# Kernel optimization log

Hardware: AMD Instinct MI355X
Metric: run time of the kernel (lower is better)

Reference implementation:

```python
import jax, jax.numpy as jnp
import numpy as np

N, D, H = 8192, 256, 128
KEEP_RATIO = 0.5
TEMP = 1.0
COS_EPS = 1e-4  # torch CosineSimilarity eps
NEG = -9e15


def setup_inputs() -> dict:
    key = jax.random.key(0)
    k1, k2, k3, k4 = jax.random.split(key, 4)
    features = jax.random.normal(k1, (N, D), dtype=jnp.float32)
    adj = jax.random.randint(k2, (N, N), 0, 2, dtype=jnp.int32)
    # module init: Linear weights ~ N(0, 0.001)
    Wq = jax.random.normal(k3, (H, D), dtype=jnp.float32) * 0.001
    Wk = jax.random.normal(k4, (H, D), dtype=jnp.float32) * 0.001
    return {"features": features, "adj": adj, "Wq": Wq, "Wk": Wk}


def _cos_normalize(x):
    # torch cosine: x / max(||x||, eps)
    n = jnp.linalg.norm(x, axis=-1, keepdims=True)
    return x / jnp.maximum(n, COS_EPS)


def reference(features, adj, Wq, Wk):
    # projections [N, H]
    Qn = _cos_normalize(features @ Wq.T)
    Kn = _cos_normalize(features @ Wk.T)
    # raw_att[i, j] = cos(Wq f_j, Wk f_i)  -> [N, N]
    raw_att = Kn @ Qn.T
    att = jnp.where(adj > 0, raw_att, NEG) * TEMP
    att = jax.nn.softmax(att, axis=1)
    prop_fea = att @ features  # [N, D]
    # nodes with no neighbors keep their own features
    adj_mask = (jnp.sum(adj, axis=1) > 0).astype(features.dtype)[:, None]
    prop_fea = adj_mask * prop_fea + (1.0 - adj_mask) * features
    # gate=None branch: fixed keep_ratio mixing
    return (1.0 - KEEP_RATIO) * prop_fea + KEEP_RATIO * features
```

## Files before the change

kernel.cpp:

```cpp
#include <hip/hip_runtime.h>
#include <stdint.h>
#include <stddef.h>

#define NN 8192
#define DD 256
#define HH 128

typedef short bf16x8  __attribute__((ext_vector_type(8)));
typedef float f32x4   __attribute__((ext_vector_type(4)));
typedef float f32x16  __attribute__((ext_vector_type(16)));
typedef int   i32x4   __attribute__((ext_vector_type(4)));

static __device__ __forceinline__ short f2bf(float x){
  unsigned u = __float_as_uint(x);
  u = (u + 0x7FFFu + ((u >> 16) & 1u)) >> 16;
  return (short)(unsigned short)u;
}
static __device__ __forceinline__ bf16x8 cvt8(const float* p){
  f32x4 a = *(const f32x4*)p;
  f32x4 b = *(const f32x4*)(p + 4);
  bf16x8 o;
  o[0]=f2bf(a[0]); o[1]=f2bf(a[1]); o[2]=f2bf(a[2]); o[3]=f2bf(a[3]);
  o[4]=f2bf(b[0]); o[5]=f2bf(b[1]); o[6]=f2bf(b[2]); o[7]=f2bf(b[3]);
  return o;
}
static __device__ __forceinline__ bf16x8 ld16(const void* p){
  i32x4 v = *(const i32x4*)p;
  return __builtin_bit_cast(bf16x8, v);
}

__global__ __launch_bounds__(256) void k_ftfrag(const float* __restrict__ f,
                                                unsigned short* __restrict__ ftf){
  int t = threadIdx.x;
  int fr = blockIdx.x * 4 + (t >> 6);
  int l  = t & 63;
  int jt = fr >> 3, dt = fr & 7;
  int j = jt * 16 + (l >> 5) * 8, d = dt * 32 + (l & 31);
  bf16x8 o;
  #pragma unroll
  for (int e = 0; e < 8; ++e) o[e] = f2bf(f[(size_t)(j + e) * DD + d]);
  *(bf16x8*)(ftf + (size_t)fr * 512 + l * 8) = o;
}

__global__ __launch_bounds__(256) void k_proj(const float* __restrict__ f,
                                              const float* __restrict__ Wq,
                                              const float* __restrict__ Wk,
                                              unsigned short* __restrict__ Qnf,
                                              unsigned short* __restrict__ Kn){
  int t = threadIdx.x, wave = t >> 6, l = t & 63;
  int i0 = blockIdx.x * 64 + wave * 16;
  int lr = l & 15, lk = l >> 4;
  bf16x8 ka[8];
  #pragma unroll
  for (int ks = 0; ks < 8; ++ks)
    ka[ks] = cvt8(f + (size_t)(i0 + lr) * DD + ks * 32 + lk * 8);
  for (int pj = 0; pj < 2; ++pj){
    const float* W = pj ? Wk : Wq;
    f32x4 acc[8];
    #pragma unroll
    for (int n = 0; n < 8; ++n) acc[n] = (f32x4){0.f,0.f,0.f,0.f};
    for (int ks = 0; ks < 8; ++ks)
      #pragma unroll
      for (int n = 0; n < 8; ++n){
        bf16x8 bb = cvt8(W + (size_t)(n * 16 + lr) * DD + ks * 32 + lk * 8);
        acc[n] = __builtin_amdgcn_mfma_f32_16x16x32_bf16(ka[ks], bb, acc[n], 0, 0, 0);
      }
    #pragma unroll
    for (int r = 0; r < 4; ++r){
      float n2 = 0.f;
      #pragma unroll
      for (int n = 0; n < 8; ++n){ float v = acc[n][r]; n2 += v * v; }
      n2 += __shfl_xor(n2, 1); n2 += __shfl_xor(n2, 2);
      n2 += __shfl_xor(n2, 4); n2 += __shfl_xor(n2, 8);
      float s = 1.f / fmaxf(sqrtf(n2), 1e-4f);
      int row = i0 + lk * 4 + r;
      #pragma unroll
      for (int n = 0; n < 8; ++n){
        short v = f2bf(acc[n][r] * s);
        if (pj){
          Kn[(size_t)row * HH + n * 16 + lr] = (unsigned short)v;
        } else {
          size_t off = ((size_t)(row >> 5) * 8 + n) * 512
                     + ((row & 31) + 32 * (lr >> 3)) * 8 + (lr & 7);
          Qnf[off] = (unsigned short)v;
        }
      }
    }
  }
}

#define STEP(CUR, NXT, SS) {                                                      \
  const int j0 = jbase + (SS) * 64;                                               \
  const int jn = ((SS) < 31) ? j0 + 64 : j0;                                      \
  _Pragma("unroll")                                                               \
  for (int r = 0; r < 16; ++r)                                                    \
    NXT[r] = __builtin_nontemporal_load(                                          \
        adj + (size_t)(iA + (r & 3) + 8 * (r >> 2)) * NN + jn + jg * 32 + lc);    \
  f32x16 st;                                                                      \
  _Pragma("unroll") for (int e = 0; e < 16; ++e) st[e] = 0.f;                     \
  { const unsigned short* qb = Qnf + ((size_t)((j0 + jg * 32) >> 5) * 8) * 512 + (size_t)l * 8; \
    _Pragma("unroll")                                                             \
    for (int hs = 0; hs < 8; ++hs)                                                \
      st = __builtin_amdgcn_mfma_f32_32x32x16_bf16(kb[hs], ld16(qb + hs * 512), st, 0, 0, 0); } \
  bf16x8 bv[8];                                                                   \
  { const unsigned short* fb = ftf + ((size_t)(j0 >> 4) * 8 + wq * 2) * 512 + (size_t)l * 8; \
    _Pragma("unroll")                                                             \
    for (int ks = 0; ks < 4; ++ks){                                               \
      bv[ks * 2]     = ld16(fb + ks * 4096);                                      \
      bv[ks * 2 + 1] = ld16(fb + ks * 4096 + 512); } }                            \
  _Pragma("unroll")                                                               \
  for (int r = 0; r < 16; ++r){                                                   \
    float wv = (CUR[r] > 0) ? __expf(st[r]) : 0.f;          \
    dacc[r] += wv;                                                                \
    int row = ig * 32 + (r & 3) + 8 * (r >> 2) + 4 * h;                           \
    int byo = row * 128 + (((jg * 32 + lc) * 2) ^ ((row & 7) << 4));              \
    *(unsigned short*)(p_lds + byo) = (unsigned short)f2bf(wv);                   \
  }                                                                               \
  __syncthreads();                                                                \
  _Pragma("unroll")                                                               \
  for (int ks = 0; ks < 4; ++ks){                                                 \
    int ko = (ks * 32 + h * 16) ^ ((lc & 7) << 4);                                \
    bf16x8 pa0 = ld16(p_lds + lc * 128 + ko);                                     \
    bf16x8 pa1 = ld16(p_lds + (32 + lc) * 128 + ko);                              \
    pv00 = __builtin_amdgcn_mfma_f32_32x32x16_bf16(pa0, bv[ks*2],   pv00, 0,0,0); \
    pv01 = __builtin_amdgcn_mfma_f32_32x32x16_bf16(pa0, bv[ks*2+1], pv01, 0,0,0); \
    pv10 = __builtin_amdgcn_mfma_f32_32x32x16_bf16(pa1, bv[ks*2],   pv10, 0,0,0); \
    pv11 = __builtin_amdgcn_mfma_f32_32x32x16_bf16(pa1, bv[ks*2+1], pv11, 0,0,0); \
  }                                                                               \
  __syncthreads();                                                                \
}

__global__ __launch_bounds__(256, 2) void k_attn(
      const int* __restrict__ adj,
      const unsigned short* __restrict__ Qnf, const unsigned short* __restrict__ Kn,
      const unsigned short* __restrict__ ftf,
      float* __restrict__ num_p, float* __restrict__ den_p){
  __shared__ __attribute__((aligned(16))) char p_lds[8192];
  int t = threadIdx.x, wave = t >> 6, l = t & 63;
  int lc = l & 31, h = l >> 5;
  int ig = wave >> 1, jg = wave & 1, wq = wave;
  int ib = blockIdx.x >> 2, js = blockIdx.x & 3;
  int i0 = ib * 64;
  int jbase = js * 2048;
  int iA = i0 + ig * 32 + 4 * h;

  bf16x8 kb[8];
  { const unsigned short* kp = Kn + (size_t)(i0 + ig * 32 + lc) * HH + h * 8;
    #pragma unroll
    for (int hs = 0; hs < 8; ++hs) kb[hs] = ld16(kp + hs * 16); }

  f32x16 pv00, pv01, pv10, pv11;
  #pragma unroll
  for (int e = 0; e < 16; ++e){ pv00[e]=0.f; pv01[e]=0.f; pv10[e]=0.f; pv11[e]=0.f; }
  float dacc[16];
  #pragma unroll
  for (int r = 0; r < 16; ++r) dacc[r] = 0.f;

  int adjA[16], adjB[16];
  #pragma unroll
  for (int r = 0; r < 16; ++r)
    adjA[r] = __builtin_nontemporal_load(
        adj + (size_t)(iA + (r & 3) + 8 * (r >> 2)) * NN + jbase + jg * 32 + lc);

  for (int sp = 0; sp < 16; ++sp){
    STEP(adjA, adjB, 2 * sp)
    STEP(adjB, adjA, 2 * sp + 1)
  }

  #pragma unroll
  for (int r = 0; r < 16; ++r){
    float v = dacc[r];
    v += __shfl_xor(v, 1); v += __shfl_xor(v, 2); v += __shfl_xor(v, 4);
    v += __shfl_xor(v, 8); v += __shfl_xor(v, 16);
    if (lc == 0){
      int i = i0 + ig * 32 + (r & 3) + 8 * (r >> 2) + 4 * h;
      den_p[(size_t)(js * 2 + jg) * NN + i] = v;
    }
  }
  float* np = num_p + (size_t)js * NN * DD;
  #pragma unroll
  for (int r = 0; r < 16; ++r){
    int i = i0 + (r & 3) + 8 * (r >> 2) + 4 * h;
    int d = wq * 64 + lc;
    np[(size_t)i * DD + d]             = pv00[r];
    np[(size_t)i * DD + d + 32]        = pv01[r];
    np[(size_t)(i + 32) * DD + d]      = pv10[r];
    np[(size_t)(i + 32) * DD + d + 32] = pv11[r];
  }
}

__global__ __launch_bounds__(256) void k_final(const float* __restrict__ num_p,
                                               const float* __restrict__ den_p,
                                               const float* __restrict__ f,
                                               float* __restrict__ out){
  int gid = blockIdx.x * 256 + threadIdx.x;
  int i = gid >> 6;
  f32x4 nv = (f32x4){0.f,0.f,0.f,0.f};
  float dv = 0.f;
  #pragma unroll
  for (int s = 0; s < 4; ++s)
    nv += *(const f32x4*)(num_p + (size_t)s * NN * DD + (size_t)gid * 4);
  #pragma unroll
  for (int s = 0; s < 8; ++s)
    dv += den_p[(size_t)s * NN + i];
  f32x4 fv = *(const f32x4*)(f + (size_t)gid * 4);
  f32x4 o;
  if (dv > 0.f){
    float inv = 0.5f / dv;
    o = nv * inv + fv * 0.5f;
  } else {
    o = fv;
  }
  *(f32x4*)(out + (size_t)gid * 4) = o;
}

extern "C" void kernel_launch(void* const* d_in, const int* in_sizes, int n_in,
                              void* d_out, int out_size, void* d_ws, size_t ws_size,
                              hipStream_t stream){
  (void)in_sizes; (void)n_in; (void)out_size;
  const float* feat = (const float*)d_in[0];
  const int*   adj  = (const int*)d_in[1];
  const float* Wq   = (const float*)d_in[2];
  const float* Wk   = (const float*)d_in[3];
  float* out = (float*)d_out;
  char* ws = (char*)d_ws;
  unsigned short* Qnf  = (unsigned short*)(ws);
  unsigned short* Kn   = (unsigned short*)(ws + (2u << 20));
  unsigned short* ftf  = (unsigned short*)(ws + (4u << 20));
  float*          num_p = (float*)(ws + (8u << 20));
  float*          den_p = (float*)(ws + (40u << 20));
  if (ws_size < (40u << 20) + 262144u) return;

  k_ftfrag<<<1024, 256, 0, stream>>>(feat, ftf);
  k_proj<<<128, 256, 0, stream>>>(feat, Wq, Wk, Qnf, Kn);
  k_attn<<<512, 256, 0, stream>>>(adj, Qnf, Kn, ftf, num_p, den_p);
  k_final<<<2048, 256, 0, stream>>>(num_p, den_p, feat, out);
}
```

Before: 235.6 us.

## Stage adjacency tiles through double-buffered LDS with 16-byte vector loads

Adjacency tiles are now loaded with 128-bit nontemporal vector loads by all threads in a coalesced pattern and staged through a double-buffered LDS tile. Previously each thread issued sixteen scalar 4-byte loads per step in the MFMA output layout. The Q operand is now loaded before the score MFMAs rather than inline, and the step macro becomes a plain loop. This is meant to cut load-instruction count and improve coalescing on the dominant adjacency stream (256 MB of int32). In exchange it adds 32 KB of LDS per block, which may reduce occupancy, and adds LDS read/write traffic.

Result: faster. 219.9 us (-6.7%).

```diff
diff --git a/kernel.cpp b/kernel.cpp
--- a/kernel.cpp
+++ b/kernel.cpp
@@ -89,60 +89,19 @@
   }
 }
 
-#define STEP(CUR, NXT, SS) {                                                      \
-  const int j0 = jbase + (SS) * 64;                                               \
-  const int jn = ((SS) < 31) ? j0 + 64 : j0;                                      \
-  _Pragma("unroll")                                                               \
-  for (int r = 0; r < 16; ++r)                                                    \
-    NXT[r] = __builtin_nontemporal_load(                                          \
-        adj + (size_t)(iA + (r & 3) + 8 * (r >> 2)) * NN + jn + jg * 32 + lc);    \
-  f32x16 st;                                                                      \
-  _Pragma("unroll") for (int e = 0; e < 16; ++e) st[e] = 0.f;                     \
-  { const unsigned short* qb = Qnf + ((size_t)((j0 + jg * 32) >> 5) * 8) * 512 + (size_t)l * 8; \
-    _Pragma("unroll")                                                             \
-    for (int hs = 0; hs < 8; ++hs)                                                \
-      st = __builtin_amdgcn_mfma_f32_32x32x16_bf16(kb[hs], ld16(qb + hs * 512), st, 0, 0, 0); } \
-  bf16x8 bv[8];                                                                   \
-  { const unsigned short* fb = ftf + ((size_t)(j0 >> 4) * 8 + wq * 2) * 512 + (size_t)l * 8; \
-    _Pragma("unroll")                                                             \
-    for (int ks = 0; ks < 4; ++ks){                                               \
-      bv[ks * 2]     = ld16(fb + ks * 4096);                                      \
-      bv[ks * 2 + 1] = ld16(fb + ks * 4096 + 512); } }                            \
-  _Pragma("unroll")                                                               \
-  for (int r = 0; r < 16; ++r){                                                   \
-    float wv = (CUR[r] > 0) ? __expf(st[r]) : 0.f;          \
-    dacc[r] += wv;                                                                \
-    int row = ig * 32 + (r & 3) + 8 * (r >> 2) + 4 * h;                           \
-    int byo = row * 128 + (((jg * 32 + lc) * 2) ^ ((row & 7) << 4));              \
-    *(unsigned short*)(p_lds + byo) = (unsigned short)f2bf(wv);                   \
-  }                                                                               \
-  __syncthreads();                                                                \
-  _Pragma("unroll")                                                               \
-  for (int ks = 0; ks < 4; ++ks){                                                 \
-    int ko = (ks * 32 + h * 16) ^ ((lc & 7) << 4);                                \
-    bf16x8 pa0 = ld16(p_lds + lc * 128 + ko);                                     \
-    bf16x8 pa1 = ld16(p_lds + (32 + lc) * 128 + ko);                              \
-    pv00 = __builtin_amdgcn_mfma_f32_32x32x16_bf16(pa0, bv[ks*2],   pv00, 0,0,0); \
-    pv01 = __builtin_amdgcn_mfma_f32_32x32x16_bf16(pa0, bv[ks*2+1], pv01, 0,0,0); \
-    pv10 = __builtin_amdgcn_mfma_f32_32x32x16_bf16(pa1, bv[ks*2],   pv10, 0,0,0); \
-    pv11 = __builtin_amdgcn_mfma_f32_32x32x16_bf16(pa1, bv[ks*2+1], pv11, 0,0,0); \
-  }                                                                               \
-  __syncthreads();                                                                \
-}
-
 __global__ __launch_bounds__(256, 2) void k_attn(
       const int* __restrict__ adj,
       const unsigned short* __restrict__ Qnf, const unsigned short* __restrict__ Kn,
       const unsigned short* __restrict__ ftf,
       float* __restrict__ num_p, float* __restrict__ den_p){
   __shared__ __attribute__((aligned(16))) char p_lds[8192];
+  __shared__ __attribute__((aligned(16))) int adj_lds[2][64][64];
   int t = threadIdx.x, wave = t >> 6, l = t & 63;
   int lc = l & 31, h = l >> 5;
   int ig = wave >> 1, jg = wave & 1, wq = wave;
   int ib = blockIdx.x >> 2, js = blockIdx.x & 3;
   int i0 = ib * 64;
   int jbase = js * 2048;
-  int iA = i0 + ig * 32 + 4 * h;
 
   bf16x8 kb[8];
   { const unsigned short* kp = Kn + (size_t)(i0 + ig * 32 + lc) * HH + h * 8;
@@ -156,15 +115,76 @@
   #pragma unroll
   for (int r = 0; r < 16; ++r) dacc[r] = 0.f;
 
-  int adjA[16], adjB[16];
-  #pragma unroll
-  for (int r = 0; r < 16; ++r)
-    adjA[r] = __builtin_nontemporal_load(
-        adj + (size_t)(iA + (r & 3) + 8 * (r >> 2)) * NN + jbase + jg * 32 + lc);
-
-  for (int sp = 0; sp < 16; ++sp){
-    STEP(adjA, adjB, 2 * sp)
-    STEP(adjB, adjA, 2 * sp + 1)
+  int arow = wave * 16 + (l >> 4);
+  int acol = (l & 15) * 4;
+
+  #pragma unroll
+  for (int k4 = 0; k4 < 4; ++k4){
+    i32x4 v = __builtin_nontemporal_load(
+        (const i32x4*)(adj + (size_t)(i0 + arow + k4 * 4) * NN + jbase + acol));
+    *(i32x4*)&adj_lds[0][arow + k4 * 4][acol] = v;
+  }
+  __syncthreads();
+
+  for (int s = 0; s < 32; ++s){
+    int j0 = jbase + s * 64;
+    int cur = s & 1, nxt = cur ^ 1;
+
+    bf16x8 qv[8];
+    { const unsigned short* qb = Qnf + ((size_t)((j0 + jg * 32) >> 5) * 8) * 512 + (size_t)l * 8;
+      #pragma unroll
+      for (int hs = 0; hs < 8; ++hs) qv[hs] = ld16(qb + hs * 512); }
+
+    i32x4 av[4];
+    if (s < 31){
+      #pragma unroll
+      for (int k4 = 0; k4 < 4; ++k4)
+        av[k4] = __builtin_nontemporal_load(
+            (const i32x4*)(adj + (size_t)(i0 + arow + k4 * 4) * NN + j0 + 64 + acol));
+    }
+
+    bf16x8 bv[8];
+    { const unsigned short* fb = ftf + ((size_t)(j0 >> 4) * 8 + wq * 2) * 512 + (size_t)l * 8;
+      #pragma unroll
+      for (int ks = 0; ks < 4; ++ks){
+        bv[ks * 2]     = ld16(fb + ks * 4096);
+        bv[ks * 2 + 1] = ld16(fb + ks * 4096 + 512); } }
+
+    f32x16 st;
+    #pragma unroll
+    for (int e = 0; e < 16; ++e) st[e] = 0.f;
+    #pragma unroll
+    for (int hs = 0; hs < 8; ++hs)
+      st = __builtin_amdgcn_mfma_f32_32x32x16_bf16(kb[hs], qv[hs], st, 0, 0, 0);
+
+    #pragma unroll
+    for (int r = 0; r < 16; ++r){
+      int row = ig * 32 + (r & 3) + 8 * (r >> 2) + 4 * h;
+      int a = adj_lds[cur][row][jg * 32 + lc];
+      float wv = (a > 0) ? __expf(st[r]) : 0.f;
+      dacc[r] += wv;
+      int byo = row * 128 + (((jg * 32 + lc) * 2) ^ ((row & 7) << 4));
+      *(unsigned short*)(p_lds + byo) = (unsigned short)f2bf(wv);
+    }
+    __syncthreads();
+
+    if (s < 31){
+      #pragma unroll
+      for (int k4 = 0; k4 < 4; ++k4)
+        *(i32x4*)&adj_lds[nxt][arow + k4 * 4][acol] = av[k4];
+    }
+
+    #pragma unroll
+    for (int ks = 0; ks < 4; ++ks){
+      int ko = (ks * 32 + h * 16) ^ ((lc & 7) << 4);
+      bf16x8 pa0 = ld16(p_lds + lc * 128 + ko);
+      bf16x8 pa1 = ld16(p_lds + (32 + lc) * 128 + ko);
+      pv00 = __builtin_amdgcn_mfma_f32_32x32x16_bf16(pa0, bv[ks*2],   pv00, 0,0,0);
+      pv01 = __builtin_amdgcn_mfma_f32_32x32x16_bf16(pa0, bv[ks*2+1], pv01, 0,0,0);
+      pv10 = __builtin_amdgcn_mfma_f32_32x32x16_bf16(pa1, bv[ks*2],   pv10, 0,0,0);
+      pv11 = __builtin_amdgcn_mfma_f32_32x32x16_bf16(pa1, bv[ks*2+1], pv11, 0,0,0);
+    }
+    __syncthreads();
   }
 
   #pragma unroll
```

## Stage adjacency and Kn through LDS, prefetch Q fragments, fuse prep kernels

Applied to the files above, without the earlier changes.

The attention kernel now loads adjacency tiles with 16-byte vector loads into a double-buffered LDS tile instead of scalar per-lane loads, and moves Kn into swizzled LDS rather than holding it in registers. Q fragments for the next step are prefetched into registers. The ftf conversion and projection kernels are merged into one launch, with the W tiles staged through LDS. Together these cut global load instruction count and one launch, at the cost of more LDS use (about 56KB per block), which may hurt the two-blocks-per-CU occupancy.

Measured after the change: 203.8 us. 13.5% less time.

```diff
diff --git a/kernel.cpp b/kernel.cpp
--- a/kernel.cpp
+++ b/kernel.cpp
@@ -29,25 +29,25 @@
   return __builtin_bit_cast(bf16x8, v);
 }
 
-__global__ __launch_bounds__(256) void k_ftfrag(const float* __restrict__ f,
-                                                unsigned short* __restrict__ ftf){
-  int t = threadIdx.x;
-  int fr = blockIdx.x * 4 + (t >> 6);
-  int l  = t & 63;
-  int jt = fr >> 3, dt = fr & 7;
-  int j = jt * 16 + (l >> 5) * 8, d = dt * 32 + (l & 31);
-  bf16x8 o;
-  #pragma unroll
-  for (int e = 0; e < 8; ++e) o[e] = f2bf(f[(size_t)(j + e) * DD + d]);
-  *(bf16x8*)(ftf + (size_t)fr * 512 + l * 8) = o;
-}
-
-__global__ __launch_bounds__(256) void k_proj(const float* __restrict__ f,
+__global__ __launch_bounds__(256) void k_prep(const float* __restrict__ f,
                                               const float* __restrict__ Wq,
                                               const float* __restrict__ Wk,
+                                              unsigned short* __restrict__ ftf,
                                               unsigned short* __restrict__ Qnf,
                                               unsigned short* __restrict__ Kn){
-  int t = threadIdx.x, wave = t >> 6, l = t & 63;
+  __shared__ unsigned short wb[128][40];
+  int t = threadIdx.x, l = t & 63;
+  {
+    int fr = blockIdx.x * 4 + (t >> 6);
+    int jt = fr >> 3, dt = fr & 7;
+    int j = jt * 16 + (l >> 5) * 8, d = dt * 32 + (l & 31);
+    bf16x8 o;
+    #pragma unroll
+    for (int e = 0; e < 8; ++e) o[e] = f2bf(f[(size_t)(j + e) * DD + d]);
+    *(bf16x8*)(ftf + (size_t)fr * 512 + l * 8) = o;
+  }
+  if (blockIdx.x >= 128) return;
+  int wave = t >> 6;
   int i0 = blockIdx.x * 64 + wave * 16;
   int lr = l & 15, lk = l >> 4;
   bf16x8 ka[8];
@@ -59,12 +59,20 @@
     f32x4 acc[8];
     #pragma unroll
     for (int n = 0; n < 8; ++n) acc[n] = (f32x4){0.f,0.f,0.f,0.f};
-    for (int ks = 0; ks < 8; ++ks)
+    for (int ks = 0; ks < 8; ++ks){
+      __syncthreads();
+      { int row = t >> 1, c0 = (t & 1) * 16;
+        const float* wp = W + (size_t)row * DD + ks * 32 + c0;
+        bf16x8 w0 = cvt8(wp), w1 = cvt8(wp + 8);
+        *(bf16x8*)&wb[row][c0]     = w0;
+        *(bf16x8*)&wb[row][c0 + 8] = w1; }
+      __syncthreads();
       #pragma unroll
       for (int n = 0; n < 8; ++n){
-        bf16x8 bb = cvt8(W + (size_t)(n * 16 + lr) * DD + ks * 32 + lk * 8);
+        bf16x8 bb = ld16(&wb[n * 16 + lr][lk * 8]);
         acc[n] = __builtin_amdgcn_mfma_f32_16x16x32_bf16(ka[ks], bb, acc[n], 0, 0, 0);
       }
+    }
     #pragma unroll
     for (int r = 0; r < 4; ++r){
       float n2 = 0.f;
@@ -89,34 +97,51 @@
   }
 }
 
-#define STEP(CUR, NXT, SS) {                                                      \
-  const int j0 = jbase + (SS) * 64;                                               \
-  const int jn = ((SS) < 31) ? j0 + 64 : j0;                                      \
-  _Pragma("unroll")                                                               \
-  for (int r = 0; r < 16; ++r)                                                    \
-    NXT[r] = __builtin_nontemporal_load(                                          \
-        adj + (size_t)(iA + (r & 3) + 8 * (r >> 2)) * NN + jn + jg * 32 + lc);    \
-  f32x16 st;                                                                      \
-  _Pragma("unroll") for (int e = 0; e < 16; ++e) st[e] = 0.f;                     \
-  { const unsigned short* qb = Qnf + ((size_t)((j0 + jg * 32) >> 5) * 8) * 512 + (size_t)l * 8; \
-    _Pragma("unroll")                                                             \
-    for (int hs = 0; hs < 8; ++hs)                                                \
-      st = __builtin_amdgcn_mfma_f32_32x32x16_bf16(kb[hs], ld16(qb + hs * 512), st, 0, 0, 0); } \
+#define STEPX(CUR, NXT, QA, QB, S) {                                              \
+  const int j0 = jbase + (S) * 64;                                                \
+  const int jn = ((S) < 31) ? j0 + 64 : jbase;                                    \
+                       \
+  i32x4 av0 = __builtin_nontemporal_load((const i32x4*)(adj + (size_t)(i0 + arow) * NN + jn + acol));      \
+  i32x4 av1 = __builtin_nontemporal_load((const i32x4*)(adj + (size_t)(i0 + arow + 4) * NN + jn + acol));  \
+  i32x4 av2 = __builtin_nontemporal_load((const i32x4*)(adj + (size_t)(i0 + arow + 8) * NN + jn + acol));  \
+  i32x4 av3 = __builtin_nontemporal_load((const i32x4*)(adj + (size_t)(i0 + arow + 12) * NN + jn + acol)); \
+                                         \
   bf16x8 bv[8];                                                                   \
   { const unsigned short* fb = ftf + ((size_t)(j0 >> 4) * 8 + wq * 2) * 512 + (size_t)l * 8; \
     _Pragma("unroll")                                                             \
     for (int ks = 0; ks < 4; ++ks){                                               \
       bv[ks * 2]     = ld16(fb + ks * 4096);                                      \
       bv[ks * 2 + 1] = ld16(fb + ks * 4096 + 512); } }                            \
+                      \
+  f32x16 st;                                                                      \
+  _Pragma("unroll") for (int e = 0; e < 16; ++e) st[e] = 0.f;                     \
+  _Pragma("unroll")                                                               \
+  for (int hs = 0; hs < 8; ++hs){                                                 \
+    bf16x8 kv = ld16(kn_lds + klrow * 256 + ((hs * 32 + h * 16) ^ kswz));         \
+    st = __builtin_amdgcn_mfma_f32_32x32x16_bf16(kv, QA[hs], st, 0, 0, 0);        \
+  }                                                                               \
+        \
+  { const unsigned short* qp = Qnf + ((size_t)((jn + jg * 32) >> 5) * 8) * 512 + (size_t)l * 8; \
+    _Pragma("unroll")                                                             \
+    for (int hs = 0; hs < 8; ++hs) QB[hs] = ld16(qp + hs * 512); }                \
+                                            \
   _Pragma("unroll")                                                               \
   for (int r = 0; r < 16; ++r){                                                   \
-    float wv = (CUR[r] > 0) ? __expf(st[r]) : 0.f;          \
+    int row = ig * 32 + (r & 3) + 8 * (r >> 2) + 4 * h;                           \
+    int a = *(const int*)(adj_lds + (CUR) * 16384 + row * 256 + (jg * 32 + lc) * 4); \
+    float wv = (a > 0) ? __expf(st[r]) : 0.f;               \
     dacc[r] += wv;                                                                \
-    int row = ig * 32 + (r & 3) + 8 * (r >> 2) + 4 * h;                           \
     int byo = row * 128 + (((jg * 32 + lc) * 2) ^ ((row & 7) << 4));              \
     *(unsigned short*)(p_lds + byo) = (unsigned short)f2bf(wv);                   \
   }                                                                               \
-  __syncthreads();                                                                \
+  asm volatile("s_waitcnt lgkmcnt(0)" ::: "memory");   \
+  __builtin_amdgcn_s_barrier();                                                   \
+        \
+  *(i32x4*)(adj_lds + (NXT) * 16384 + arow * 256 + acol * 4)        = av0;        \
+  *(i32x4*)(adj_lds + (NXT) * 16384 + (arow + 4) * 256 + acol * 4)  = av1;        \
+  *(i32x4*)(adj_lds + (NXT) * 16384 + (arow + 8) * 256 + acol * 4)  = av2;        \
+  *(i32x4*)(adj_lds + (NXT) * 16384 + (arow + 12) * 256 + acol * 4) = av3;        \
+                                                    \
   _Pragma("unroll")                                                               \
   for (int ks = 0; ks < 4; ++ks){                                                 \
     int ko = (ks * 32 + h * 16) ^ ((lc & 7) << 4);                                \
@@ -127,7 +152,8 @@
     pv10 = __builtin_amdgcn_mfma_f32_32x32x16_bf16(pa1, bv[ks*2],   pv10, 0,0,0); \
     pv11 = __builtin_amdgcn_mfma_f32_32x32x16_bf16(pa1, bv[ks*2+1], pv11, 0,0,0); \
   }                                                                               \
-  __syncthreads();                                                                \
+  asm volatile("s_waitcnt lgkmcnt(0)" ::: "memory");   \
+  __builtin_amdgcn_s_barrier();                                                   \
 }
 
 __global__ __launch_bounds__(256, 2) void k_attn(
@@ -136,18 +162,25 @@
       const unsigned short* __restrict__ ftf,
       float* __restrict__ num_p, float* __restrict__ den_p){
   __shared__ __attribute__((aligned(16))) char p_lds[8192];
+  __shared__ __attribute__((aligned(16))) char adj_lds[32768];
+  __shared__ __attribute__((aligned(16))) char kn_lds[16384];
   int t = threadIdx.x, wave = t >> 6, l = t & 63;
   int lc = l & 31, h = l >> 5;
   int ig = wave >> 1, jg = wave & 1, wq = wave;
   int ib = blockIdx.x >> 2, js = blockIdx.x & 3;
   int i0 = ib * 64;
   int jbase = js * 2048;
-  int iA = i0 + ig * 32 + 4 * h;
-
-  bf16x8 kb[8];
-  { const unsigned short* kp = Kn + (size_t)(i0 + ig * 32 + lc) * HH + h * 8;
-    #pragma unroll
-    for (int hs = 0; hs < 8; ++hs) kb[hs] = ld16(kp + hs * 16); }
+  int klrow = ig * 32 + lc, kswz = (lc & 7) << 4;
+  int arow = wave * 16 + (l >> 4);
+  int acol = (l & 15) * 4;
+
+  { int row = t >> 2;
+    const unsigned short* kp = Kn + (size_t)(i0 + row) * HH + (t & 3) * 32;
+    #pragma unroll
+    for (int q = 0; q < 4; ++q){
+      i32x4 v = *(const i32x4*)(kp + q * 8);
+      *(i32x4*)(kn_lds + row * 256 + (((t & 3) * 64 + q * 16) ^ ((row & 7) << 4))) = v;
+    } }
 
   f32x16 pv00, pv01, pv10, pv11;
   #pragma unroll
@@ -156,15 +189,24 @@
   #pragma unroll
   for (int r = 0; r < 16; ++r) dacc[r] = 0.f;
 
-  int adjA[16], adjB[16];
-  #pragma unroll
-  for (int r = 0; r < 16; ++r)
-    adjA[r] = __builtin_nontemporal_load(
-        adj + (size_t)(iA + (r & 3) + 8 * (r >> 2)) * NN + jbase + jg * 32 + lc);
+  bf16x8 qa[8], qb[8];
+  { i32x4 a0 = __builtin_nontemporal_load((const i32x4*)(adj + (size_t)(i0 + arow) * NN + jbase + acol));
+    i32x4 a1 = __builtin_nontemporal_load((const i32x4*)(adj + (size_t)(i0 + arow + 4) * NN + jbase + acol));
+    i32x4 a2 = __builtin_nontemporal_load((const i32x4*)(adj + (size_t)(i0 + arow + 8) * NN + jbase + acol));
+    i32x4 a3 = __builtin_nontemporal_load((const i32x4*)(adj + (size_t)(i0 + arow + 12) * NN + jbase + acol));
+    const unsigned short* qp = Qnf + ((size_t)((jbase + jg * 32) >> 5) * 8) * 512 + (size_t)l * 8;
+    #pragma unroll
+    for (int hs = 0; hs < 8; ++hs) qa[hs] = ld16(qp + hs * 512);
+    *(i32x4*)(adj_lds + arow * 256 + acol * 4)        = a0;
+    *(i32x4*)(adj_lds + (arow + 4) * 256 + acol * 4)  = a1;
+    *(i32x4*)(adj_lds + (arow + 8) * 256 + acol * 4)  = a2;
+    *(i32x4*)(adj_lds + (arow + 12) * 256 + acol * 4) = a3;
+  }
+  __syncthreads();
 
   for (int sp = 0; sp < 16; ++sp){
-    STEP(adjA, adjB, 2 * sp)
-    STEP(adjB, adjA, 2 * sp + 1)
+    STEPX(0, 1, qa, qb, 2 * sp)
+    STEPX(1, 0, qb, qa, 2 * sp + 1)
   }
 
   #pragma unroll
@@ -224,15 +266,14 @@
   const float* Wk   = (const float*)d_in[3];
   float* out = (float*)d_out;
   char* ws = (char*)d_ws;
-  unsigned short* Qnf  = (unsigned short*)(ws);
-  unsigned short* Kn   = (unsigned short*)(ws + (2u << 20));
-  unsigned short* ftf  = (unsigned short*)(ws + (4u << 20));
+  unsigned short* Qnf   = (unsigned short*)(ws);
+  unsigned short* Kn    = (unsigned short*)(ws + (2u << 20));
+  unsigned short* ftf   = (unsigned short*)(ws + (4u << 20));
   float*          num_p = (float*)(ws + (8u << 20));
   float*          den_p = (float*)(ws + (40u << 20));
   if (ws_size < (40u << 20) + 262144u) return;
 
-  k_ftfrag<<<1024, 256, 0, stream>>>(feat, ftf);
-  k_proj<<<128, 256, 0, stream>>>(feat, Wq, Wk, Qnf, Kn);
+  k_prep<<<1024, 256, 0, stream>>>(feat, Wq, Wk, ftf, Qnf, Kn);
   k_attn<<<512, 256, 0, stream>>>(adj, Qnf, Kn, ftf, num_p, den_p);
   k_final<<<2048, 256, 0, stream>>>(num_p, den_p, feat, out);
 }
```
